# Kernel optimization log

Measured on AMD Instinct MI355X. Metric: run time of the kernel, lower is better.

Reference implementation:

```python
import jax, jax.numpy as jnp
import numpy as np

BLANK = 0
B, T, U = 4, 128, 64
EPROJS, EMBED, DUNITS, JOINT, ODIM = 512, 512, 1024, 512, 2048


def lstm_cell(x, h, c, W_ih, W_hh, b_ih, b_hh):
    # PyTorch LSTMCell: gates ordered (i, f, g, o)
    gates = x @ W_ih.T + b_ih + h @ W_hh.T + b_hh
    i, f, g, o = jnp.split(gates, 4, axis=-1)
    c_new = jax.nn.sigmoid(f) * c + jax.nn.sigmoid(i) * jnp.tanh(g)
    h_new = jax.nn.sigmoid(o) * jnp.tanh(c_new)
    return h_new, c_new


def setup_inputs() -> dict:
    key = jax.random.key(0)
    ks = jax.random.split(key, 20)
    s = 0.05
    embed = jax.random.normal(ks[2], (ODIM, EMBED)) * s
    embed = embed.at[BLANK].set(0.0)  # padding_idx
    return {
        'hs_pad': jax.random.normal(ks[0], (B, T, EPROJS)),
        'ys_in_pad': jax.random.randint(ks[1], (B, U), 0, ODIM, dtype=jnp.int32),
        'embed': embed,
        'W_ih0': jax.random.normal(ks[3], (4 * DUNITS, EMBED)) * s,
        'W_hh0': jax.random.normal(ks[4], (4 * DUNITS, DUNITS)) * s,
        'b_ih0': jax.random.normal(ks[5], (4 * DUNITS,)) * s,
        'b_hh0': jax.random.normal(ks[6], (4 * DUNITS,)) * s,
        'W_ih1': jax.random.normal(ks[7], (4 * DUNITS, DUNITS)) * s,
        'W_hh1': jax.random.normal(ks[8], (4 * DUNITS, DUNITS)) * s,
        'b_ih1': jax.random.normal(ks[9], (4 * DUNITS,)) * s,
        'b_hh1': jax.random.normal(ks[10], (4 * DUNITS,)) * s,
        'W_enc': jax.random.normal(ks[11], (JOINT, EPROJS)) * s,
        'b_enc': jax.random.normal(ks[12], (JOINT,)) * s,
        'W_dec': jax.random.normal(ks[13], (JOINT, DUNITS)) * s,
        'W_out': jax.random.normal(ks[14], (ODIM, JOINT)) * s,
        'b_out': jax.random.normal(ks[15], (ODIM,)) * s,
    }


def reference(hs_pad, ys_in_pad, embed, W_ih0, W_hh0, b_ih0, b_hh0,
              W_ih1, W_hh1, b_ih1, b_hh1, W_enc, b_enc, W_dec, W_out, b_out):
    # Embedding with padding_idx=blank (blank row contributes zero).
    eys = embed[ys_in_pad] * (ys_in_pad != BLANK)[..., None].astype(embed.dtype)  # (B,U,E)

    def step(carry, ey):
        h0, c0, h1, c1 = carry
        h0, c0 = lstm_cell(ey, h0, c0, W_ih0, W_hh0, b_ih0, b_hh0)
        h1, c1 = lstm_cell(h0, h1, c1, W_ih1, W_hh1, b_ih1, b_hh1)
        return (h0, c0, h1, c1), h1

    z0 = jnp.zeros((hs_pad.shape[0], DUNITS), hs_pad.dtype)
    _, hs = jax.lax.scan(step, (z0, z0, z0, z0), jnp.swapaxes(eys, 0, 1))
    h_dec = jnp.swapaxes(hs, 0, 1)  # (B,U,Hdec)

    # Joint network: broadcast-add + tanh + output projection.
    enc_p = jnp.einsum('bte,je->btj', hs_pad, W_enc) + b_enc   # (B,T,J)
    dec_p = jnp.einsum('bud,jd->buj', h_dec, W_dec)            # (B,U,J)
    z = jnp.tanh(enc_p[:, :, None, :] + dec_p[:, None, :, :])  # (B,T,U,J)
    return jnp.einsum('btuj,oj->btuo', z, W_out) + b_out       # (B,T,U,odim)
```

## Files before the change

kernel.cpp:

```cpp
#include <hip/hip_runtime.h>
#include <stdint.h>

typedef short bf16x8 __attribute__((ext_vector_type(8)));
typedef float f32x4 __attribute__((ext_vector_type(4)));
typedef unsigned int u32x4 __attribute__((ext_vector_type(4)));

__device__ __forceinline__ unsigned short f2bf(float f) {
  union { float f; unsigned int i; } v; v.f = f;
  unsigned int r = v.i + 0x7FFF + ((v.i >> 16) & 1);
  return (unsigned short)(r >> 16);
}
__device__ __forceinline__ float bfu2f(unsigned short u) {
  union { unsigned int i; float f; } v; v.i = ((unsigned int)u) << 16; return v.f;
}
__device__ __forceinline__ void gload_lds16(const void* g, void* l) {
  __builtin_amdgcn_global_load_lds(
      (const __attribute__((address_space(1))) unsigned int*)g,
      (__attribute__((address_space(3))) unsigned int*)l,
      16, 0, 0);
}
__device__ __forceinline__ void store16_coh(unsigned int* p, u32x4 v) {
  asm volatile("global_store_dwordx4 %0, %1, off sc0 sc1" :: "v"(p), "v"(v) : "memory");
}
__device__ __forceinline__ void spin_load6(const unsigned int* p0, const unsigned int* p1,
                                           const unsigned int* p2, const unsigned int* p3,
                                           const unsigned int* p4, const unsigned int* p5,
                                           u32x4& r0, u32x4& r1, u32x4& r2,
                                           u32x4& r3, u32x4& r4, u32x4& r5) {
  asm volatile(
      "global_load_dwordx4 %0, %6, off sc0 sc1\n\t"
      "global_load_dwordx4 %1, %7, off sc0 sc1\n\t"
      "global_load_dwordx4 %2, %8, off sc0 sc1\n\t"
      "global_load_dwordx4 %3, %9, off sc0 sc1\n\t"
      "global_load_dwordx4 %4, %10, off sc0 sc1\n\t"
      "global_load_dwordx4 %5, %11, off sc0 sc1\n\t"
      "s_waitcnt vmcnt(0)"
      : "=&v"(r0), "=&v"(r1), "=&v"(r2), "=&v"(r3), "=&v"(r4), "=&v"(r5)
      : "v"(p0), "v"(p1), "v"(p2), "v"(p3), "v"(p4), "v"(p5)
      : "memory");
}
__device__ __forceinline__ void spin_load3p(const unsigned int* p0, const unsigned int* p1,
                                            const unsigned int* p2, const unsigned int* pp,
                                            u32x4& r0, u32x4& r1, u32x4& r2, unsigned int& pt) {
  asm volatile(
      "global_load_dwordx4 %0, %4, off sc0 sc1\n\t"
      "global_load_dwordx4 %1, %5, off sc0 sc1\n\t"
      "global_load_dwordx4 %2, %6, off sc0 sc1\n\t"
      "global_load_dword %3, %7, off sc0 sc1\n\t"
      "s_waitcnt vmcnt(0)"
      : "=&v"(r0), "=&v"(r1), "=&v"(r2), "=&v"(pt)
      : "v"(p0), "v"(p1), "v"(p2), "v"(pp)
      : "memory");
}

__global__ __launch_bounds__(256) void k_cvtprep(const float* __restrict__ s0, const float* __restrict__ s1,
                                                 const float* __restrict__ s2, const float* __restrict__ s3,
                                                 unsigned short* __restrict__ d0, unsigned short* __restrict__ d1,
                                                 unsigned short* __restrict__ d2, unsigned short* __restrict__ d3,
                                                 const int* __restrict__ ys,
                                                 const float* __restrict__ embed,
                                                 float* __restrict__ eys,
                                                 unsigned int* __restrict__ exch) {
  if (blockIdx.x < 6656) {
    int j = blockIdx.x * 256 + threadIdx.x;
    const float* s; unsigned short* d; int o;
    if (j < 524288)       { s = s0; d = d0; o = j; }
    else if (j < 1048576) { s = s1; d = d1; o = j - 524288; }
    else if (j < 1572864) { s = s2; d = d2; o = j - 1048576; }
    else                  { s = s3; d = d3; o = j - 1572864; }
    size_t off = (size_t)o * 8;
    f32x4 v0 = *(const f32x4*)(s + off);
    f32x4 v1 = *(const f32x4*)(s + off + 4);
    bf16x8 r;
#pragma unroll
    for (int k = 0; k < 4; k++) { r[k] = (short)f2bf(v0[k]); r[4 + k] = (short)f2bf(v1[k]); }
    *(bf16x8*)(d + off) = r;
  } else {
    int idx = (blockIdx.x - 6656) * 256 + threadIdx.x;
    int row = idx >> 6;
    int e = (idx & 63) * 8;
    int y = ys[row];
    f32x4 v0 = {0.f, 0.f, 0.f, 0.f}, v1 = {0.f, 0.f, 0.f, 0.f};
    if (y != 0) {
      v0 = *(const f32x4*)(embed + (size_t)y * 512 + e);
      v1 = *(const f32x4*)(embed + (size_t)y * 512 + e + 4);
    }
    *(f32x4*)(eys + (size_t)row * 512 + e) = v0;
    *(f32x4*)(eys + (size_t)row * 512 + e + 4) = v1;
    exch[idx] = 0u;
    exch[idx + 16384] = 0u;
  }
}

__global__ __launch_bounds__(256) void k_gemm_bias(const float* __restrict__ A,
                                                   const float* __restrict__ W,
                                                   const float* __restrict__ b1,
                                                   const float* __restrict__ b2,
                                                   void* __restrict__ Cout, int obf,
                                                   int M, int N, int K) {
  __shared__ unsigned short Als[64][40];
  __shared__ unsigned short Wls[64][40];
  int tid = threadIdx.x;
  int lane = tid & 63, wid = tid >> 6;
  int mtiles = M >> 6;
  int mt = blockIdx.x % mtiles, nt = blockIdx.x / mtiles;
  int srow = tid >> 2, sseg = tid & 3;
  f32x4 acc[4];
#pragma unroll
  for (int nf = 0; nf < 4; nf++) acc[nf] = (f32x4){0.f, 0.f, 0.f, 0.f};

  for (int kc = 0; kc < K; kc += 32) {
    const float* ap = A + (size_t)(mt * 64 + srow) * K + kc + sseg * 8;
    const float* wp = W + (size_t)(nt * 64 + srow) * K + kc + sseg * 8;
    f32x4 a0 = *(const f32x4*)ap, a1 = *(const f32x4*)(ap + 4);
    f32x4 w0 = *(const f32x4*)wp, w1 = *(const f32x4*)(wp + 4);
    bf16x8 av, wv;
#pragma unroll
    for (int k = 0; k < 4; k++) {
      av[k] = (short)f2bf(a0[k]); av[4 + k] = (short)f2bf(a1[k]);
      wv[k] = (short)f2bf(w0[k]); wv[4 + k] = (short)f2bf(w1[k]);
    }
    __syncthreads();
    *(bf16x8*)(&Als[srow][sseg * 8]) = av;
    *(bf16x8*)(&Wls[srow][sseg * 8]) = wv;
    __syncthreads();
    bf16x8 af = *(const bf16x8*)(&Als[wid * 16 + (lane & 15)][(lane >> 4) * 8]);
#pragma unroll
    for (int nf = 0; nf < 4; nf++) {
      bf16x8 bf = *(const bf16x8*)(&Wls[nf * 16 + (lane & 15)][(lane >> 4) * 8]);
      acc[nf] = __builtin_amdgcn_mfma_f32_16x16x32_bf16(af, bf, acc[nf], 0, 0, 0);
    }
  }
  int rloc = (lane >> 4) * 4;
  int col0 = lane & 15;
#pragma unroll
  for (int nf = 0; nf < 4; nf++) {
    int n = nt * 64 + nf * 16 + col0;
    float bias = 0.f;
    if (b1) bias += b1[n];
    if (b2) bias += b2[n];
#pragma unroll
    for (int r = 0; r < 4; r++) {
      int m = mt * 64 + wid * 16 + rloc + r;
      float v = acc[nf][r] + bias;
      if (obf) ((unsigned short*)Cout)[(size_t)m * N + n] = f2bf(v);
      else     ((float*)Cout)[(size_t)m * N + n] = v;
    }
  }
}

__global__ __launch_bounds__(512) void k_lstm_fused(
    const float* __restrict__ X0,
    float* __restrict__ hdec,
    const unsigned short* __restrict__ W_hh0,
    const unsigned short* __restrict__ W_ih1,
    const unsigned short* __restrict__ W_hh1,
    const float* __restrict__ b_ih1,
    const float* __restrict__ b_hh1,
    unsigned int* __restrict__ exch) {
  __shared__ unsigned short X_lds[4][2064];
  __shared__ float red[8][4][16][4];
  int tid = threadIdx.x;
  int lane = tid & 63, w = tid >> 6;
  bool isL1 = blockIdx.x >= 64;
  int bidl = blockIdx.x & 63;
  int base = bidl * 16;
  unsigned int* REC0 = exch;
  unsigned int* REC1 = exch + 16384;

  bf16x8 wf[4][8];
  int ch = lane & 15;
  int klo = (lane >> 4) << 3;
  int kb = isL1 ? w * 256 : w * 128;
#pragma unroll
  for (int nt = 0; nt < 4; nt++) {
    int grow = nt * 1024 + base + ch;
    if (!isL1) {
#pragma unroll
      for (int ks = 0; ks < 4; ks++)
        wf[nt][ks] = *(const bf16x8*)(W_hh0 + (size_t)grow * 1024 + kb + ks * 32 + klo);
    } else {
#pragma unroll
      for (int ks = 0; ks < 8; ks++) {
        int k = kb + ks * 32 + klo;
        const unsigned short* src = (k < 1024) ? (W_ih1 + (size_t)grow * 1024 + k)
                                               : (W_hh1 + (size_t)grow * 1024 + (k - 1024));
        wf[nt][ks] = *(const bf16x8*)src;
      }
    }
  }

  float creg = 0.f;
  float bs0 = 0.f, bs1 = 0.f, bs2 = 0.f, bs3 = 0.f;
  int gch = tid >> 2, gb = tid & 3;
  if (isL1 && tid < 64) {
    int c = base + gch;
    bs0 = b_ih1[c] + b_hh1[c];
    bs1 = b_ih1[1024 + c] + b_hh1[1024 + c];
    bs2 = b_ih1[2048 + c] + b_hh1[2048 + c];
    bs3 = b_ih1[3072 + c] + b_hh1[3072 + c];
  }

  int uoff[3], upb[3], us[3]; bool uneed[3];
#pragma unroll
  for (int r = 0; r < 3; r++) {
    int u = tid + r * 512;
    uneed[r] = (u < 1408);
    int uc = uneed[r] ? u : 1407;
    int pb = uc / 22;
    int s = uc - pb * 22;
    upb[r] = pb; us[r] = s;
    uoff[r] = pb * 128 + s * 4;
  }

#define STAGE_UNIT(rv, rr, off1024)                                           \
  if (uneed[rv]) {                                                            \
    int pb_ = upb[rv], s_ = us[rv];                                           \
    _Pragma("unroll")                                                         \
    for (int j_ = 0; j_ < 3; j_++) {                                          \
      int i_ = 3 * s_ + j_;                                                   \
      if (i_ < 64) {                                                          \
        union { unsigned int u; float f; } cv_; cv_.u = rr[j_];               \
        X_lds[i_ & 3][off1024 + pb_ * 16 + (i_ >> 2)] = f2bf(cv_.f);          \
      }                                                                       \
    }                                                                         \
  }

  int ar = ch & 3;
  if (!isL1) {
    for (int p = 0; p < 64; p++) {
      float xp0 = 0.f, xp1 = 0.f, xp2 = 0.f, xp3 = 0.f;
      if (tid < 64) {
        const float* x0p = X0 + ((size_t)(gb * 64 + p)) * 4096 + base + gch;
        xp0 = x0p[0]; xp1 = x0p[1024]; xp2 = x0p[2048]; xp3 = x0p[3072];
      }
      {
        unsigned int* b0 = REC0 + (unsigned)(p & 1) * 8192;
        const unsigned int* pp = REC1 + (unsigned)((p - 1) & 1) * 8192 + (tid & 63) * 128 + 3;
        unsigned expP = (p == 0) ? 0u : (unsigned)(p - 1);
        u32x4 r0, r1, r2; unsigned int pt;
        while (true) {
          spin_load3p(b0 + uoff[0], b0 + uoff[1], b0 + uoff[2], pp, r0, r1, r2, pt);
          bool ok = (!uneed[0] || r0[3] == (unsigned)p) && (!uneed[1] || r1[3] == (unsigned)p) &&
                    (!uneed[2] || r2[3] == (unsigned)p) && (pt >= expP);
          if (ok) break;
          __builtin_amdgcn_s_sleep(1);
        }
        STAGE_UNIT(0, r0, 0) STAGE_UNIT(1, r1, 0) STAGE_UNIT(2, r2, 0)
      }
      __syncthreads();
      {
        f32x4 acc[4];
#pragma unroll
        for (int nt = 0; nt < 4; nt++) acc[nt] = (f32x4){0.f, 0.f, 0.f, 0.f};
#pragma unroll
        for (int ks = 0; ks < 4; ks++) {
          bf16x8 a = *(const bf16x8*)&X_lds[ar][kb + ks * 32 + klo];
#pragma unroll
          for (int nt = 0; nt < 4; nt++)
            acc[nt] = __builtin_amdgcn_mfma_f32_16x16x32_bf16(a, wf[nt][ks], acc[nt], 0, 0, 0);
        }
        if (lane < 16) {
#pragma unroll
          for (int nt = 0; nt < 4; nt++) *(f32x4*)&red[w][nt][lane][0] = acc[nt];
        }
      }
      __syncthreads();
      if (tid < 64) {
        float g0 = 0.f, g1 = 0.f, g2 = 0.f, g3 = 0.f;
#pragma unroll
        for (int w8 = 0; w8 < 8; w8++) {
          g0 += red[w8][0][gch][gb]; g1 += red[w8][1][gch][gb];
          g2 += red[w8][2][gch][gb]; g3 += red[w8][3][gch][gb];
        }
        g0 += xp0; g1 += xp1; g2 += xp2; g3 += xp3;
        float ii = 1.f / (1.f + __expf(-g0));
        float ff = 1.f / (1.f + __expf(-g1));
        float oo = 1.f / (1.f + __expf(-g3));
        float cn = ff * creg + ii * tanhf(g2);
        creg = cn;
        float hn = oo * tanhf(cn);
        int l = tid;
        float v0 = __shfl(hn, 3 * l);
        float v1 = __shfl(hn, 3 * l + 1);
        float v2 = __shfl(hn, 3 * l + 2);
        if (l < 22) {
          unsigned tag = (unsigned)(p + 1);
          unsigned int* rec = REC0 + (tag & 1) * 8192 + bidl * 128 + l * 4;
          u32x4 d;
          d[0] = __float_as_uint(v0); d[1] = __float_as_uint(v1);
          d[2] = __float_as_uint(v2); d[3] = tag;
          store16_coh(rec, d);
        }
      }
    }
  } else {
    for (int p = 1; p <= 64; p++) {
      {
        unsigned int* b0 = REC0 + (unsigned)(p & 1) * 8192;
        unsigned int* b1 = REC1 + (unsigned)((p - 1) & 1) * 8192;
        u32x4 r0, r1, r2, r3, r4, r5;
        unsigned exp0 = (unsigned)p, exp1 = (unsigned)(p - 1);
        while (true) {
          spin_load6(b0 + uoff[0], b0 + uoff[1], b0 + uoff[2],
                     b1 + uoff[0], b1 + uoff[1], b1 + uoff[2],
                     r0, r1, r2, r3, r4, r5);
          bool ok = (!uneed[0] || (r0[3] == exp0 && r3[3] == exp1)) &&
                    (!uneed[1] || (r1[3] == exp0 && r4[3] == exp1)) &&
                    (!uneed[2] || (r2[3] == exp0 && r5[3] == exp1));
          if (ok) break;
          __builtin_amdgcn_s_sleep(1);
        }
        STAGE_UNIT(0, r0, 0) STAGE_UNIT(1, r1, 0) STAGE_UNIT(2, r2, 0)
        STAGE_UNIT(0, r3, 1024) STAGE_UNIT(1, r4, 1024) STAGE_UNIT(2, r5, 1024)
      }
      __syncthreads();
      {
        f32x4 acc[4];
#pragma unroll
        for (int nt = 0; nt < 4; nt++) acc[nt] = (f32x4){0.f, 0.f, 0.f, 0.f};
#pragma unroll
        for (int ks = 0; ks < 8; ks++) {
          bf16x8 a = *(const bf16x8*)&X_lds[ar][kb + ks * 32 + klo];
#pragma unroll
          for (int nt = 0; nt < 4; nt++)
            acc[nt] = __builtin_amdgcn_mfma_f32_16x16x32_bf16(a, wf[nt][ks], acc[nt], 0, 0, 0);
        }
        if (lane < 16) {
#pragma unroll
          for (int nt = 0; nt < 4; nt++) *(f32x4*)&red[w][nt][lane][0] = acc[nt];
        }
      }
      __syncthreads();
      if (tid < 64) {
        float g0 = 0.f, g1 = 0.f, g2 = 0.f, g3 = 0.f;
#pragma unroll
        for (int w8 = 0; w8 < 8; w8++) {
          g0 += red[w8][0][gch][gb]; g1 += red[w8][1][gch][gb];
          g2 += red[w8][2][gch][gb]; g3 += red[w8][3][gch][gb];
        }
        g0 += bs0; g1 += bs1; g2 += bs2; g3 += bs3;
        float ii = 1.f / (1.f + __expf(-g0));
        float ff = 1.f / (1.f + __expf(-g1));
        float oo = 1.f / (1.f + __expf(-g3));
        float cn = ff * creg + ii * tanhf(g2);
        creg = cn;
        float hn = oo * tanhf(cn);
        hdec[((size_t)(gb * 64 + (p - 1))) * 1024 + base + gch] = hn;
        int l = tid;
        float v0 = __shfl(hn, 3 * l);
        float v1 = __shfl(hn, 3 * l + 1);
        float v2 = __shfl(hn, 3 * l + 2);
        if (l < 22) {
          unsigned tag = (unsigned)p;
          unsigned int* rec = REC1 + (tag & 1) * 8192 + bidl * 128 + l * 4;
          u32x4 d;
          d[0] = __float_as_uint(v0); d[1] = __float_as_uint(v1);
          d[2] = __float_as_uint(v2); d[3] = tag;
          store16_coh(rec, d);
        }
      }
    }
  }
#undef STAGE_UNIT
}

__global__ __launch_bounds__(256) void k_z(const unsigned short* __restrict__ encpb,
                                           const unsigned short* __restrict__ decpb,
                                           unsigned short* __restrict__ Z) {
  int idx = blockIdx.x * 256 + threadIdx.x;
  int m = idx >> 6;
  int k0 = (idx & 63) * 8;
  int bt = m >> 6;
  int b = m >> 13, u = m & 63;
  bf16x8 ev = *(const bf16x8*)(encpb + (size_t)bt * 512 + k0);
  bf16x8 dv = *(const bf16x8*)(decpb + (size_t)(b * 64 + u) * 512 + k0);
  bf16x8 r;
#pragma unroll
  for (int j = 0; j < 8; j++) {
    float x = bfu2f((unsigned short)ev[j]) + bfu2f((unsigned short)dv[j]);
    float e = __expf(x + x);
    r[j] = (short)f2bf(1.f - 2.f / (e + 1.f));
  }
  *(bf16x8*)(Z + (size_t)m * 512 + k0) = r;
}

__global__ __launch_bounds__(512, 2) void k_gemm_out(const unsigned short* __restrict__ Z,
                                                     const unsigned short* __restrict__ Wout,
                                                     const float* __restrict__ bout,
                                                     float* __restrict__ out) {
  __shared__ unsigned short Wls[8][8192];
  int tid = threadIdx.x;
  int lane = tid & 63, wid = tid >> 6;
  int bid = blockIdx.x;
  int mpart = bid & 15, ngroup = bid >> 4;

#pragma unroll
  for (int kc = 0; kc < 8; kc++) {
    unsigned short* dst = &Wls[kc][0];
#pragma unroll
    for (int q = 0; q < 2; q++) {
      int idx = tid + q * 512;
      int n = idx >> 3, sl = idx & 7;
      int ss = sl ^ (n & 7);
      gload_lds16(Wout + (size_t)(ngroup * 128 + n) * 512 + kc * 64 + ss * 8, dst + idx * 8);
    }
  }
  float bb[8];
#pragma unroll
  for (int nf = 0; nf < 8; nf++) bb[nf] = bout[ngroup * 128 + nf * 16 + (lane & 15)];
  asm volatile("s_waitcnt vmcnt(0)" ::: "memory");
  __syncthreads();

  int rowwave = mpart * 2048 + wid * 256;
  int ocol0 = ngroup * 128;
  for (int mg = 0; mg < 4; mg++) {
    int rowbase = rowwave + mg * 64;
    f32x4 acc[4][8];
#pragma unroll
    for (int mf = 0; mf < 4; mf++)
#pragma unroll
      for (int nf = 0; nf < 8; nf++) acc[mf][nf] = (f32x4){0.f, 0.f, 0.f, 0.f};

#pragma unroll
    for (int ks = 0; ks < 16; ks++) {
      bf16x8 a[4];
#pragma unroll
      for (int mf = 0; mf < 4; mf++) {
        int r = rowbase + mf * 16 + (lane & 15);
        a[mf] = *(const bf16x8*)(Z + (size_t)r * 512 + ks * 32 + ((lane >> 4) << 3));
      }
      const unsigned short* Wb = &Wls[ks >> 1][0];
      int slot = (ks & 1) * 4 + (lane >> 4);
#pragma unroll
      for (int nf = 0; nf < 8; nf++) {
        int nl = nf * 16 + (lane & 15);
        int phys = slot ^ (nl & 7);
        bf16x8 bfr = *(const bf16x8*)(Wb + nl * 64 + phys * 8);
#pragma unroll
        for (int mf = 0; mf < 4; mf++)
          acc[mf][nf] = __builtin_amdgcn_mfma_f32_16x16x32_bf16(a[mf], bfr, acc[mf][nf], 0, 0, 0);
      }
    }
#pragma unroll
    for (int mf = 0; mf < 4; mf++) {
      int rb = rowbase + mf * 16 + ((lane >> 4) << 2);
#pragma unroll
      for (int nf = 0; nf < 8; nf++) {
        int o = ocol0 + nf * 16 + (lane & 15);
        float bias = bb[nf];
#pragma unroll
        for (int q = 0; q < 4; q++)
          __builtin_nontemporal_store(acc[mf][nf][q] + bias, &out[(size_t)(rb + q) * 2048 + o]);
      }
    }
  }
}

extern "C" void kernel_launch(void* const* d_in, const int* in_sizes, int n_in,
                              void* d_out, int out_size, void* d_ws, size_t ws_size,
                              hipStream_t stream) {
  const float* hs   = (const float*)d_in[0];
  const int*   ys   = (const int*)d_in[1];
  const float* emb  = (const float*)d_in[2];
  const float* Wih0 = (const float*)d_in[3];
  const float* Whh0 = (const float*)d_in[4];
  const float* bih0 = (const float*)d_in[5];
  const float* bhh0 = (const float*)d_in[6];
  const float* Wih1 = (const float*)d_in[7];
  const float* Whh1 = (const float*)d_in[8];
  const float* bih1 = (const float*)d_in[9];
  const float* bhh1 = (const float*)d_in[10];
  const float* Wenc = (const float*)d_in[11];
  const float* benc = (const float*)d_in[12];
  const float* Wdec = (const float*)d_in[13];
  const float* Wout = (const float*)d_in[14];
  const float* bout = (const float*)d_in[15];

  char* ws = (char*)d_ws;
  unsigned short* Woutb = (unsigned short*)(ws + 0);
  unsigned short* encpb = (unsigned short*)(ws + 2097152);
  unsigned short* decpb = (unsigned short*)(ws + 2621440);
  unsigned int*   exch  = (unsigned int*)(ws + 2883584);
  unsigned short* Z     = (unsigned short*)(ws + 3031040);
  float*          eys   = (float*)(ws + 3031040);
  float*          X0    = (float*)(ws + 3555328);
  float*          hdec  = (float*)(ws + 7749632);
  unsigned short* Whh0b = (unsigned short*)(ws + 8798208);
  unsigned short* Wih1b = (unsigned short*)(ws + 17186816);
  unsigned short* Whh1b = (unsigned short*)(ws + 25575424);
  float*          out   = (float*)d_out;

  k_cvtprep<<<6720, 256, 0, stream>>>(Whh0, Wih1, Whh1, Wout, Whh0b, Wih1b, Whh1b, Woutb,
                                      ys, emb, eys, exch);
  k_gemm_bias<<<256, 256, 0, stream>>>(eys, Wih0, bih0, bhh0, X0, 0, 256, 4096, 512);
  k_gemm_bias<<<64, 256, 0, stream>>>(hs, Wenc, benc, nullptr, encpb, 1, 512, 512, 512);
  k_lstm_fused<<<128, 512, 0, stream>>>(X0, hdec, Whh0b, Wih1b, Whh1b, bih1, bhh1, exch);
  k_gemm_bias<<<32, 256, 0, stream>>>(hdec, Wdec, nullptr, nullptr, decpb, 1, 256, 512, 1024);
  k_z<<<8192, 256, 0, stream>>>(encpb, decpb, Z);
  k_gemm_out<<<256, 512, 0, stream>>>(Z, Woutb, bout, out);
}
```

Baseline: 419.6 us.

## Fuse layer-0 input projection GEMM into the persistent LSTM kernel prologue

```diff
diff --git a/kernel.cpp b/kernel.cpp
--- a/kernel.cpp
+++ b/kernel.cpp
@@ -150,7 +150,10 @@
 }
 
 __global__ __launch_bounds__(512) void k_lstm_fused(
-    const float* __restrict__ X0,
+    const float* __restrict__ eys,
+    const float* __restrict__ Wih0,
+    const float* __restrict__ b_ih0,
+    const float* __restrict__ b_hh0,
     float* __restrict__ hdec,
     const unsigned short* __restrict__ W_hh0,
     const unsigned short* __restrict__ W_ih1,
@@ -160,6 +163,7 @@
     unsigned int* __restrict__ exch) {
   __shared__ unsigned short X_lds[4][2064];
   __shared__ float red[8][4][16][4];
+  __shared__ float G_lds[256][66];
   int tid = threadIdx.x;
   int lane = tid & 63, w = tid >> 6;
   bool isL1 = blockIdx.x >= 64;
@@ -168,10 +172,55 @@
   unsigned int* REC0 = exch;
   unsigned int* REC1 = exch + 16384;
 
-  bf16x8 wf[4][8];
   int ch = lane & 15;
   int klo = (lane >> 4) << 3;
   int kb = isL1 ? w * 256 : w * 128;
+
+  if (!isL1) {
+    bf16x8 bfr[4][16];
+#pragma unroll
+    for (int nt = 0; nt < 4; nt++) {
+      const float* wp = Wih0 + (size_t)(nt * 1024 + base + ch) * 512;
+#pragma unroll
+      for (int ks = 0; ks < 16; ks++) {
+        int k0 = ks * 32 + klo;
+        f32x4 w0 = *(const f32x4*)(wp + k0);
+        f32x4 w1 = *(const f32x4*)(wp + k0 + 4);
+        bf16x8 v;
+#pragma unroll
+        for (int j = 0; j < 4; j++) { v[j] = (short)f2bf(w0[j]); v[4 + j] = (short)f2bf(w1[j]); }
+        bfr[nt][ks] = v;
+      }
+    }
+#pragma unroll
+    for (int rep = 0; rep < 2; rep++) {
+      int mt = w + rep * 8;
+      bf16x8 afr[16];
+      const float* ap = eys + (size_t)(mt * 16 + ch) * 512;
+#pragma unroll
+      for (int ks = 0; ks < 16; ks++) {
+        int k0 = ks * 32 + klo;
+        f32x4 a0 = *(const f32x4*)(ap + k0);
+        f32x4 a1 = *(const f32x4*)(ap + k0 + 4);
+        bf16x8 v;
+#pragma unroll
+        for (int j = 0; j < 4; j++) { v[j] = (short)f2bf(a0[j]); v[4 + j] = (short)f2bf(a1[j]); }
+        afr[ks] = v;
+      }
+#pragma unroll
+      for (int nt = 0; nt < 4; nt++) {
+        f32x4 acc = (f32x4){0.f, 0.f, 0.f, 0.f};
+#pragma unroll
+        for (int ks = 0; ks < 16; ks++)
+          acc = __builtin_amdgcn_mfma_f32_16x16x32_bf16(afr[ks], bfr[nt][ks], acc, 0, 0, 0);
+#pragma unroll
+        for (int q = 0; q < 4; q++)
+          G_lds[mt * 16 + (lane >> 4) * 4 + q][nt * 16 + ch] = acc[q];
+      }
+    }
+  }
+
+  bf16x8 wf[4][8];
 #pragma unroll
   for (int nt = 0; nt < 4; nt++) {
     int grow = nt * 1024 + base + ch;
@@ -193,12 +242,14 @@
   float creg = 0.f;
   float bs0 = 0.f, bs1 = 0.f, bs2 = 0.f, bs3 = 0.f;
   int gch = tid >> 2, gb = tid & 3;
-  if (isL1 && tid < 64) {
+  if (tid < 64) {
     int c = base + gch;
-    bs0 = b_ih1[c] + b_hh1[c];
-    bs1 = b_ih1[1024 + c] + b_hh1[1024 + c];
-    bs2 = b_ih1[2048 + c] + b_hh1[2048 + c];
-    bs3 = b_ih1[3072 + c] + b_hh1[3072 + c];
+    const float* bi = isL1 ? b_ih1 : b_ih0;
+    const float* bh = isL1 ? b_hh1 : b_hh0;
+    bs0 = bi[c] + bh[c];
+    bs1 = bi[1024 + c] + bh[1024 + c];
+    bs2 = bi[2048 + c] + bh[2048 + c];
+    bs3 = bi[3072 + c] + bh[3072 + c];
   }
 
   int uoff[3], upb[3], us[3]; bool uneed[3];
@@ -228,12 +279,8 @@
 
   int ar = ch & 3;
   if (!isL1) {
+    __syncthreads();
     for (int p = 0; p < 64; p++) {
-      float xp0 = 0.f, xp1 = 0.f, xp2 = 0.f, xp3 = 0.f;
-      if (tid < 64) {
-        const float* x0p = X0 + ((size_t)(gb * 64 + p)) * 4096 + base + gch;
-        xp0 = x0p[0]; xp1 = x0p[1024]; xp2 = x0p[2048]; xp3 = x0p[3072];
-      }
       {
         unsigned int* b0 = REC0 + (unsigned)(p & 1) * 8192;
         const unsigned int* pp = REC1 + (unsigned)((p - 1) & 1) * 8192 + (tid & 63) * 128 + 3;
@@ -273,7 +320,11 @@
           g0 += red[w8][0][gch][gb]; g1 += red[w8][1][gch][gb];
           g2 += red[w8][2][gch][gb]; g3 += red[w8][3][gch][gb];
         }
-        g0 += xp0; g1 += xp1; g2 += xp2; g3 += xp3;
+        int grow = gb * 64 + p;
+        g0 += G_lds[grow][gch] + bs0;
+        g1 += G_lds[grow][16 + gch] + bs1;
+        g2 += G_lds[grow][32 + gch] + bs2;
+        g3 += G_lds[grow][48 + gch] + bs3;
         float ii = 1.f / (1.f + __expf(-g0));
         float ff = 1.f / (1.f + __expf(-g1));
         float oo = 1.f / (1.f + __expf(-g3));
@@ -484,7 +535,6 @@
   unsigned int*   exch  = (unsigned int*)(ws + 2883584);
   unsigned short* Z     = (unsigned short*)(ws + 3031040);
   float*          eys   = (float*)(ws + 3031040);
-  float*          X0    = (float*)(ws + 3555328);
   float*          hdec  = (float*)(ws + 7749632);
   unsigned short* Whh0b = (unsigned short*)(ws + 8798208);
   unsigned short* Wih1b = (unsigned short*)(ws + 17186816);
@@ -493,9 +543,9 @@
 
   k_cvtprep<<<6720, 256, 0, stream>>>(Whh0, Wih1, Whh1, Wout, Whh0b, Wih1b, Whh1b, Woutb,
                                       ys, emb, eys, exch);
-  k_gemm_bias<<<256, 256, 0, stream>>>(eys, Wih0, bih0, bhh0, X0, 0, 256, 4096, 512);
   k_gemm_bias<<<64, 256, 0, stream>>>(hs, Wenc, benc, nullptr, encpb, 1, 512, 512, 512);
-  k_lstm_fused<<<128, 512, 0, stream>>>(X0, hdec, Whh0b, Wih1b, Whh1b, bih1, bhh1, exch);
+  k_lstm_fused<<<128, 512, 0, stream>>>(eys, Wih0, bih0, bhh0, hdec,
+                                        Whh0b, Wih1b, Whh1b, bih1, bhh1, exch);
   k_gemm_bias<<<32, 256, 0, stream>>>(hdec, Wdec, nullptr, nullptr, decpb, 1, 256, 512, 1024);
   k_z<<<8192, 256, 0, stream>>>(encpb, decpb, Z);
   k_gemm_out<<<256, 512, 0, stream>>>(Z, Woutb, bout, out);
```

Result: slower. 487.5 us (+16.2%).

## Fuse LSTM weight bf16 conversion into register preload and embedding gather into X0 GEMM

Applied to the files above, without the earlier changes.

```diff
diff --git a/kernel.cpp b/kernel.cpp
--- a/kernel.cpp
+++ b/kernel.cpp
@@ -12,6 +12,14 @@
 }
 __device__ __forceinline__ float bfu2f(unsigned short u) {
   union { unsigned int i; float f; } v; v.i = ((unsigned int)u) << 16; return v.f;
+}
+__device__ __forceinline__ bf16x8 cvt8(const float* p) {
+  f32x4 a = *(const f32x4*)p;
+  f32x4 b = *(const f32x4*)(p + 4);
+  bf16x8 r;
+#pragma unroll
+  for (int j = 0; j < 4; j++) { r[j] = (short)f2bf(a[j]); r[4 + j] = (short)f2bf(b[j]); }
+  return r;
 }
 __device__ __forceinline__ void gload_lds16(const void* g, void* l) {
   __builtin_amdgcn_global_load_lds(
@@ -53,42 +61,64 @@
       : "memory");
 }
 
-__global__ __launch_bounds__(256) void k_cvtprep(const float* __restrict__ s0, const float* __restrict__ s1,
-                                                 const float* __restrict__ s2, const float* __restrict__ s3,
-                                                 unsigned short* __restrict__ d0, unsigned short* __restrict__ d1,
-                                                 unsigned short* __restrict__ d2, unsigned short* __restrict__ d3,
-                                                 const int* __restrict__ ys,
-                                                 const float* __restrict__ embed,
-                                                 float* __restrict__ eys,
+__global__ __launch_bounds__(256) void k_cvtprep(const float* __restrict__ Wout,
+                                                 unsigned short* __restrict__ Woutb,
                                                  unsigned int* __restrict__ exch) {
-  if (blockIdx.x < 6656) {
+  if (blockIdx.x < 512) {
     int j = blockIdx.x * 256 + threadIdx.x;
-    const float* s; unsigned short* d; int o;
-    if (j < 524288)       { s = s0; d = d0; o = j; }
-    else if (j < 1048576) { s = s1; d = d1; o = j - 524288; }
-    else if (j < 1572864) { s = s2; d = d2; o = j - 1048576; }
-    else                  { s = s3; d = d3; o = j - 1572864; }
-    size_t off = (size_t)o * 8;
-    f32x4 v0 = *(const f32x4*)(s + off);
-    f32x4 v1 = *(const f32x4*)(s + off + 4);
-    bf16x8 r;
-#pragma unroll
-    for (int k = 0; k < 4; k++) { r[k] = (short)f2bf(v0[k]); r[4 + k] = (short)f2bf(v1[k]); }
-    *(bf16x8*)(d + off) = r;
+    size_t off = (size_t)j * 8;
+    *(bf16x8*)(Woutb + off) = cvt8(Wout + off);
   } else {
-    int idx = (blockIdx.x - 6656) * 256 + threadIdx.x;
-    int row = idx >> 6;
-    int e = (idx & 63) * 8;
-    int y = ys[row];
-    f32x4 v0 = {0.f, 0.f, 0.f, 0.f}, v1 = {0.f, 0.f, 0.f, 0.f};
-    if (y != 0) {
-      v0 = *(const f32x4*)(embed + (size_t)y * 512 + e);
-      v1 = *(const f32x4*)(embed + (size_t)y * 512 + e + 4);
-    }
-    *(f32x4*)(eys + (size_t)row * 512 + e) = v0;
-    *(f32x4*)(eys + (size_t)row * 512 + e + 4) = v1;
+    int idx = (blockIdx.x - 512) * 256 + threadIdx.x;
     exch[idx] = 0u;
     exch[idx + 16384] = 0u;
+  }
+}
+
+__global__ __launch_bounds__(256) void k_gemm_x0(const int* __restrict__ ys,
+                                                 const float* __restrict__ embed,
+                                                 const float* __restrict__ W,
+                                                 const float* __restrict__ b1,
+                                                 const float* __restrict__ b2,
+                                                 float* __restrict__ C) {
+  const int N = 4096, K = 512;
+  __shared__ unsigned short Als[64][40];
+  __shared__ unsigned short Wls[64][40];
+  int tid = threadIdx.x;
+  int lane = tid & 63, wid = tid >> 6;
+  int mt = blockIdx.x & 3, nt = blockIdx.x >> 2;
+  int srow = tid >> 2, sseg = tid & 3;
+  int y = ys[mt * 64 + srow];
+  f32x4 acc[4];
+#pragma unroll
+  for (int nf = 0; nf < 4; nf++) acc[nf] = (f32x4){0.f, 0.f, 0.f, 0.f};
+
+  for (int kc = 0; kc < K; kc += 32) {
+    bf16x8 av = {};
+    if (y != 0) av = cvt8(embed + (size_t)y * K + kc + sseg * 8);
+    bf16x8 wv = cvt8(W + (size_t)(nt * 64 + srow) * K + kc + sseg * 8);
+    __syncthreads();
+    *(bf16x8*)(&Als[srow][sseg * 8]) = av;
+    *(bf16x8*)(&Wls[srow][sseg * 8]) = wv;
+    __syncthreads();
+    bf16x8 af = *(const bf16x8*)(&Als[wid * 16 + (lane & 15)][(lane >> 4) * 8]);
+#pragma unroll
+    for (int nf = 0; nf < 4; nf++) {
+      bf16x8 bf = *(const bf16x8*)(&Wls[nf * 16 + (lane & 15)][(lane >> 4) * 8]);
+      acc[nf] = __builtin_amdgcn_mfma_f32_16x16x32_bf16(af, bf, acc[nf], 0, 0, 0);
+    }
+  }
+  int rloc = (lane >> 4) * 4;
+  int col0 = lane & 15;
+#pragma unroll
+  for (int nf = 0; nf < 4; nf++) {
+    int n = nt * 64 + nf * 16 + col0;
+    float bias = b1[n] + b2[n];
+#pragma unroll
+    for (int r = 0; r < 4; r++) {
+      int m = mt * 64 + wid * 16 + rloc + r;
+      C[(size_t)m * N + n] = acc[nf][r] + bias;
+    }
   }
 }
 
@@ -110,16 +140,8 @@
   for (int nf = 0; nf < 4; nf++) acc[nf] = (f32x4){0.f, 0.f, 0.f, 0.f};
 
   for (int kc = 0; kc < K; kc += 32) {
-    const float* ap = A + (size_t)(mt * 64 + srow) * K + kc + sseg * 8;
-    const float* wp = W + (size_t)(nt * 64 + srow) * K + kc + sseg * 8;
-    f32x4 a0 = *(const f32x4*)ap, a1 = *(const f32x4*)(ap + 4);
-    f32x4 w0 = *(const f32x4*)wp, w1 = *(const f32x4*)(wp + 4);
-    bf16x8 av, wv;
-#pragma unroll
-    for (int k = 0; k < 4; k++) {
-      av[k] = (short)f2bf(a0[k]); av[4 + k] = (short)f2bf(a1[k]);
-      wv[k] = (short)f2bf(w0[k]); wv[4 + k] = (short)f2bf(w1[k]);
-    }
+    bf16x8 av = cvt8(A + (size_t)(mt * 64 + srow) * K + kc + sseg * 8);
+    bf16x8 wv = cvt8(W + (size_t)(nt * 64 + srow) * K + kc + sseg * 8);
     __syncthreads();
     *(bf16x8*)(&Als[srow][sseg * 8]) = av;
     *(bf16x8*)(&Wls[srow][sseg * 8]) = wv;
@@ -152,9 +174,9 @@
 __global__ __launch_bounds__(512) void k_lstm_fused(
     const float* __restrict__ X0,
     float* __restrict__ hdec,
-    const unsigned short* __restrict__ W_hh0,
-    const unsigned short* __restrict__ W_ih1,
-    const unsigned short* __restrict__ W_hh1,
+    const float* __restrict__ Whh0f,
+    const float* __restrict__ Wih1f,
+    const float* __restrict__ Whh1f,
     const float* __restrict__ b_ih1,
     const float* __restrict__ b_hh1,
     unsigned int* __restrict__ exch) {
@@ -178,14 +200,14 @@
     if (!isL1) {
 #pragma unroll
       for (int ks = 0; ks < 4; ks++)
-        wf[nt][ks] = *(const bf16x8*)(W_hh0 + (size_t)grow * 1024 + kb + ks * 32 + klo);
+        wf[nt][ks] = cvt8(Whh0f + (size_t)grow * 1024 + kb + ks * 32 + klo);
     } else {
 #pragma unroll
       for (int ks = 0; ks < 8; ks++) {
         int k = kb + ks * 32 + klo;
-        const unsigned short* src = (k < 1024) ? (W_ih1 + (size_t)grow * 1024 + k)
-                                               : (W_hh1 + (size_t)grow * 1024 + (k - 1024));
-        wf[nt][ks] = *(const bf16x8*)src;
+        const float* src = (k < 1024) ? (Wih1f + (size_t)grow * 1024 + k)
+                                      : (Whh1f + (size_t)grow * 1024 + (k - 1024));
+        wf[nt][ks] = cvt8(src);
       }
     }
   }
@@ -483,19 +505,14 @@
   unsigned short* decpb = (unsigned short*)(ws + 2621440);
   unsigned int*   exch  = (unsigned int*)(ws + 2883584);
   unsigned short* Z     = (unsigned short*)(ws + 3031040);
-  float*          eys   = (float*)(ws + 3031040);
   float*          X0    = (float*)(ws + 3555328);
   float*          hdec  = (float*)(ws + 7749632);
-  unsigned short* Whh0b = (unsigned short*)(ws + 8798208);
-  unsigned short* Wih1b = (unsigned short*)(ws + 17186816);
-  unsigned short* Whh1b = (unsigned short*)(ws + 25575424);
   float*          out   = (float*)d_out;
 
-  k_cvtprep<<<6720, 256, 0, stream>>>(Whh0, Wih1, Whh1, Wout, Whh0b, Wih1b, Whh1b, Woutb,
-                                      ys, emb, eys, exch);
-  k_gemm_bias<<<256, 256, 0, stream>>>(eys, Wih0, bih0, bhh0, X0, 0, 256, 4096, 512);
+  k_cvtprep<<<576, 256, 0, stream>>>(Wout, Woutb, exch);
+  k_gemm_x0<<<256, 256, 0, stream>>>(ys, emb, Wih0, bih0, bhh0, X0);
   k_gemm_bias<<<64, 256, 0, stream>>>(hs, Wenc, benc, nullptr, encpb, 1, 512, 512, 512);
-  k_lstm_fused<<<128, 512, 0, stream>>>(X0, hdec, Whh0b, Wih1b, Whh1b, bih1, bhh1, exch);
+  k_lstm_fused<<<128, 512, 0, stream>>>(X0, hdec, Whh0, Wih1, Whh1, bih1, bhh1, exch);
   k_gemm_bias<<<32, 256, 0, stream>>>(hdec, Wdec, nullptr, nullptr, decpb, 1, 256, 512, 1024);
   k_z<<<8192, 256, 0, stream>>>(encpb, decpb, Z);
   k_gemm_out<<<256, 512, 0, stream>>>(Z, Woutb, bout, out);
```

Result: slower. 436.1 us (+3.9%).
